# Optimization experiments

Measured on AMD Instinct MI355X. Metric: run time of the kernel, lower is better.

The kernel has to match this reference:

```python
import jax, jax.numpy as jnp
import numpy as np

TEMPERATURE = 0.1  # InfoNCE default
K_POS, K_NEG = 5, 10


def _l2norm(x, eps):
    return x / jnp.maximum(jnp.linalg.norm(x, axis=-1, keepdims=True), eps)


def setup_inputs() -> dict:
    key = jax.random.key(0)
    k1, k2 = jax.random.split(key)
    anchor = jax.random.normal(k1, (4096, 512), dtype=jnp.float32)
    sample = jax.random.normal(k2, (4096, 512), dtype=jnp.float32)
    return {"anchor": anchor, "sample": sample}


def reference(anchor, sample):
    N = anchor.shape[0]
    # Pairwise cosine similarity (torch.cosine_similarity eps=1e-8), computed
    a = _l2norm(anchor, 1e-8)
    sim = a @ a.T  # (N, N)

    # topk largest=True (5 nearest) and largest=False (10 farthest)
    _, pos_idx = jax.lax.top_k(sim, K_POS)    # (N, 5)
    _, neg_idx = jax.lax.top_k(-sim, K_NEG)   # (N, 10), ascending sim

    # Faithful replication of the original gather/repeat pattern:
    # query = sample.repeat(5, 1) -> tiling (index i maps to sample[i % N])
    query = jnp.tile(sample, (K_POS, 1))                          # (5N, d)
    pos = sample[pos_idx.reshape(-1)]                             # (5N, d) anchor-major
    neg = sample[neg_idx.reshape(-1)].reshape(N, K_NEG, -1)       # (N, 10, d)
    neg = jnp.repeat(neg, K_POS, axis=0)                          # (5N, 10, d)

    # InfoNCE (negative_mode='paired'): F.normalize (eps=1e-12) then logits.
    q = _l2norm(query, 1e-12)
    p = _l2norm(pos, 1e-12)
    n = _l2norm(neg, 1e-12)
    pos_logit = jnp.sum(q * p, axis=1, keepdims=True)             # (5N, 1)
    neg_logits = jnp.einsum('bd,bkd->bk', q, n)                   # (5N, 10)
    logits = jnp.concatenate([pos_logit, neg_logits], axis=1) / TEMPERATURE
    # cross_entropy with labels == 0, mean reduction
    loss = -jnp.mean(jax.nn.log_softmax(logits, axis=1)[:, 0])
    return loss
```

## Files before the change

kernel.cpp:

```cpp
#include <hip/hip_runtime.h>
#include <math.h>

#define N 4096
#define D 512
#define KPOS 5
#define KNEG 10
#define NB 32
#define NPAIR (NB * (NB - 1) / 2)
#define NJOB 1024

typedef short s16x8 __attribute__((ext_vector_type(8)));
typedef unsigned short u16x8 __attribute__((ext_vector_type(8)));
typedef float f32x4 __attribute__((ext_vector_type(4)));

__device__ __forceinline__ unsigned short f2bf(float x) {
    unsigned u = __float_as_uint(x);
    unsigned r = (u + 0x7FFFu + ((u >> 16) & 1u)) >> 16;
    return (unsigned short)r;
}
__device__ __forceinline__ float bf2f(unsigned short b) {
    return __uint_as_float(((unsigned)b) << 16);
}
__device__ __forceinline__ unsigned short mapbf(float x) {
    const unsigned short h = f2bf(x);
    return h ^ ((h & 0x8000u) ? 0xFFFFu : 0x8000u);
}
__device__ __forceinline__ unsigned umax_(unsigned a, unsigned b) { return a > b ? a : b; }
__device__ __forceinline__ unsigned umin_(unsigned a, unsigned b) { return a < b ? a : b; }

__global__ __launch_bounds__(256) void norm_kernel(const float* __restrict__ anchor,
                                                   const float* __restrict__ sample,
                                                   unsigned short* __restrict__ Abf,
                                                   unsigned short* __restrict__ s_norm) {
    const int wave = threadIdx.x >> 6, lane = threadIdx.x & 63;
    const int row = blockIdx.x * 4 + wave;
    const bool is_anchor = row < N;
    const float* in = is_anchor ? anchor + (size_t)row * D
                                : sample + (size_t)(row - N) * D;
    const float eps = is_anchor ? 1e-8f : 1e-12f;

    const float4 v0 = *(const float4*)&in[lane * 4];
    const float4 v1 = *(const float4*)&in[256 + lane * 4];
    float ss = v0.x * v0.x + v0.y * v0.y + v0.z * v0.z + v0.w * v0.w
             + v1.x * v1.x + v1.y * v1.y + v1.z * v1.z + v1.w * v1.w;
#pragma unroll
    for (int off = 32; off > 0; off >>= 1) ss += __shfl_xor(ss, off);
    const float inv = 1.0f / fmaxf(sqrtf(ss), eps);

    unsigned short* out = is_anchor ? Abf + (size_t)row * D
                                    : s_norm + (size_t)(row - N) * D;
    ushort4 o0, o1;
    o0.x = f2bf(v0.x * inv); o0.y = f2bf(v0.y * inv);
    o0.z = f2bf(v0.z * inv); o0.w = f2bf(v0.w * inv);
    o1.x = f2bf(v1.x * inv); o1.y = f2bf(v1.y * inv);
    o1.z = f2bf(v1.z * inv); o1.w = f2bf(v1.w * inv);
    *(ushort4*)&out[lane * 4] = o0;
    *(ushort4*)&out[256 + lane * 4] = o1;
}

#define ATILE (128 * 64)
#define BTILE (64 * 64)

__device__ __forceinline__ void stage_ab(const unsigned short* __restrict__ A,
                                         unsigned short* As, unsigned short* Bs,
                                         int rowA, int colB, int kl, int t) {
#pragma unroll
    for (int i = 0; i < 4; ++i) {
        const int c = i * 256 + t;
        const int r = c >> 3;
        const int ke = ((c & 7) ^ (r & 7)) * 8;
        __builtin_amdgcn_global_load_lds(
            (const __attribute__((address_space(1))) void*)(A + (size_t)(rowA + r) * D + kl + ke),
            (__attribute__((address_space(3))) void*)(As + c * 8), 16, 0, 0);
    }
#pragma unroll
    for (int i = 0; i < 2; ++i) {
        const int c = i * 256 + t;
        const int r = c >> 3;
        const int ke = ((c & 7) ^ (r & 7)) * 8;
        __builtin_amdgcn_global_load_lds(
            (const __attribute__((address_space(1))) void*)(A + (size_t)(colB + r) * D + kl + ke),
            (__attribute__((address_space(3))) void*)(Bs + c * 8), 16, 0, 0);
    }
}

__global__ __launch_bounds__(256) void gemm_bf16(const unsigned short* __restrict__ Abf,
                                                 unsigned short* __restrict__ C) {
    const int q = (blockIdx.x % 8) * (NJOB / 8) + blockIdx.x / 8;

    int bi, bj, h;
    if (q < 2 * NPAIR) {
        const int op = q >> 1;
        h = q & 1;
        bi = (int)(31.5f - sqrtf(31.5f * 31.5f - 2.f * (float)op));
        while (31 * bi - bi * (bi - 1) / 2 > op) --bi;
        while (31 * (bi + 1) - (bi + 1) * bi / 2 <= op) ++bi;
        bj = bi + 1 + (op - (31 * bi - bi * (bi - 1) / 2));
    } else {
        const int d = q - 2 * NPAIR;
        bi = bj = d >> 1;
        h = d & 1;
    }

    __shared__ __align__(16) unsigned short As[2 * ATILE];
    __shared__ __align__(16) unsigned short Bs[2 * BTILE];

    const int t = threadIdx.x;
    const int l = t & 63;
    const int w = t >> 6;
    const int wr = w >> 1, wc = w & 1;
    const int rowA = bi * 128;
    const int colB = bj * 128 + h * 64;
    const int lrow = l & 15, lgrp = l >> 4;

    f32x4 acc[4][2];
#pragma unroll
    for (int m = 0; m < 4; ++m)
#pragma unroll
        for (int n = 0; n < 2; ++n) acc[m][n] = (f32x4){0.f, 0.f, 0.f, 0.f};

    stage_ab(Abf, As, Bs, rowA, colB, 0, t);
    __syncthreads();

    for (int kc = 0; kc < 8; ++kc) {
        const int cur = kc & 1;
        if (kc < 7)
            stage_ab(Abf, As + (cur ^ 1) * ATILE, Bs + (cur ^ 1) * BTILE,
                     rowA, colB, (kc + 1) * 64, t);

        const char* AsB = (const char*)(As + cur * ATILE);
        const char* BsB = (const char*)(Bs + cur * BTILE);
#pragma unroll
        for (int kk = 0; kk < 2; ++kk) {
            s16x8 af[4], bfr[2];
#pragma unroll
            for (int m = 0; m < 4; ++m) {
                const int row = wr * 64 + m * 16 + lrow;
                af[m] = *(const s16x8*)(AsB + row * 128 + (((kk * 4 + lgrp) ^ (row & 7)) * 16));
            }
#pragma unroll
            for (int n = 0; n < 2; ++n) {
                const int row = wc * 32 + n * 16 + lrow;
                bfr[n] = *(const s16x8*)(BsB + row * 128 + (((kk * 4 + lgrp) ^ (row & 7)) * 16));
            }
#pragma unroll
            for (int m = 0; m < 4; ++m)
#pragma unroll
                for (int n = 0; n < 2; ++n)
                    acc[m][n] = __builtin_amdgcn_mfma_f32_16x16x32_bf16(af[m], bfr[n], acc[m][n], 0, 0, 0);
        }
        __syncthreads();
    }

#pragma unroll
    for (int m = 0; m < 4; ++m) {
#pragma unroll
        for (int n = 0; n < 2; ++n) {
            const int col = colB + wc * 32 + n * 16 + lrow;
            const int row0 = rowA + wr * 64 + m * 16 + lgrp * 4;
#pragma unroll
            for (int j = 0; j < 4; ++j)
                C[(size_t)(row0 + j) * N + col] = mapbf(acc[m][n][j]);
        }
    }
    if (bi != bj) {
#pragma unroll
        for (int m = 0; m < 4; ++m) {
#pragma unroll
            for (int n = 0; n < 2; ++n) {
                const int col = colB + wc * 32 + n * 16 + lrow;
                const int row0 = rowA + wr * 64 + m * 16 + lgrp * 4;
                ushort4 pk;
                pk.x = mapbf(acc[m][n][0]);
                pk.y = mapbf(acc[m][n][1]);
                pk.z = mapbf(acc[m][n][2]);
                pk.w = mapbf(acc[m][n][3]);
                *(ushort4*)&C[(size_t)col * N + row0] = pk;
            }
        }
    }
}

__device__ __forceinline__ void ins_top(unsigned* tk, unsigned c) {
#pragma unroll
    for (int q = 0; q < KPOS - 1; ++q) {
        const unsigned x = umax_(tk[q], c);
        c = umin_(tk[q], c);
        tk[q] = x;
    }
    tk[KPOS - 1] = umax_(tk[KPOS - 1], c);
}
__device__ __forceinline__ void ins_bot(unsigned* bk, unsigned c) {
#pragma unroll
    for (int q = 0; q < KNEG - 1; ++q) {
        const unsigned x = umin_(bk[q], c);
        c = umax_(bk[q], c);
        bk[q] = x;
    }
    bk[KNEG - 1] = umin_(bk[KNEG - 1], c);
}
__device__ __forceinline__ void scan8(const unsigned short* __restrict__ s,
                                      int lane, int e, unsigned* tk, unsigned* bk) {
    const int base = 8 * (lane + 64 * e);
    const u16x8 v8 = *(const u16x8*)&s[base];
#pragma unroll
    for (int j = 0; j < 8; ++j) {
        const unsigned kv = ((unsigned)v8[j]) << 16;
        const int idx = base + j;
        ins_top(tk, kv | (unsigned)(idx ^ 0xFFF));
        ins_bot(bk, kv | (unsigned)idx);
    }
}

__global__ __launch_bounds__(256) void fused_topk_loss(const unsigned short* __restrict__ sim,
                                                       const unsigned short* __restrict__ s_norm,
                                                       float* __restrict__ partials) {
    __shared__ float wsum[4];
    const int wave = threadIdx.x >> 6, lane = threadIdx.x & 63;
    const int ia = blockIdx.x * 4 + wave;
    const unsigned short* s = sim + (size_t)ia * N;
    const int cc = lane & 15;
    const int g = lane >> 4;

    unsigned tkA[KPOS], bkA[KNEG], tkB[KPOS], bkB[KNEG];
#pragma unroll
    for (int q = 0; q < KPOS; ++q) { tkA[q] = 0u; tkB[q] = 0u; }
#pragma unroll
    for (int q = 0; q < KNEG; ++q) { bkA[q] = 0xFFFFFFFFu; bkB[q] = 0xFFFFFFFFu; }

#pragma unroll
    for (int ee = 0; ee < 4; ++ee) {
        scan8(s, lane, 2 * ee, tkA, bkA);
        scan8(s, lane, 2 * ee + 1, tkB, bkB);
    }
#pragma unroll
    for (int q = 0; q < KPOS; ++q) ins_top(tkA, tkB[q]);
#pragma unroll
    for (int q = 0; q < KNEG; ++q) ins_bot(bkA, bkB[q]);

    int rowB = 0;
#pragma unroll
    for (int it = 0; it < KPOS; ++it) {
        unsigned m = tkA[0];
#pragma unroll
        for (int off = 32; off > 0; off >>= 1) m = umax_(m, (unsigned)__shfl_xor((int)m, off));
        if (cc == it) rowB = (int)((m & 0xFFFu) ^ 0xFFFu);
        if (tkA[0] == m) {
#pragma unroll
            for (int q = 0; q < KPOS - 1; ++q) tkA[q] = tkA[q + 1];
            tkA[KPOS - 1] = 0u;
        }
    }
#pragma unroll
    for (int it = 0; it < KNEG; ++it) {
        unsigned m = bkA[0];
#pragma unroll
        for (int off = 32; off > 0; off >>= 1) m = umin_(m, (unsigned)__shfl_xor((int)m, off));
        if (cc == KPOS + it) rowB = (int)(m & 0xFFFu);
        if (bkA[0] == m) {
#pragma unroll
            for (int q = 0; q < KNEG - 1; ++q) bkA[q] = bkA[q + 1];
            bkA[KNEG - 1] = 0xFFFFFFFFu;
        }
    }

    const int rowA = (ia * KPOS + ((cc < KPOS) ? cc : 0)) & (N - 1);
    const unsigned short* pA = s_norm + (size_t)rowA * D + g * 8;
    const unsigned short* pB = s_norm + (size_t)rowB * D + g * 8;

    s16x8 a[16], b[16];
#pragma unroll
    for (int kk = 0; kk < 16; ++kk) {
        a[kk] = *(const s16x8*)(pA + kk * 32);
        b[kk] = *(const s16x8*)(pB + kk * 32);
    }
    __builtin_amdgcn_sched_barrier(0);
    asm volatile("" ::: "memory");

    f32x4 acc = (f32x4){0.f, 0.f, 0.f, 0.f};
#pragma unroll
    for (int kk = 0; kk < 16; ++kk)
        acc = __builtin_amdgcn_mfma_f32_16x16x32_bf16(a[kk], b[kk], acc, 0, 0, 0);

    float lsum = 0.f;
#pragma unroll
    for (int j = 0; j < 4; ++j) {
        const int p = g * 4 + j;
        const float logit = acc[j] * 10.f;
        const bool isneg = (cc >= KPOS) && (cc < 15);
        const bool ispos = (cc == p);
        float x = (ispos || isneg) ? logit : -__builtin_inff();
        float m = x;
#pragma unroll
        for (int off = 1; off < 16; off <<= 1) m = fmaxf(m, __shfl_xor(m, off));
        float e = (ispos || isneg) ? expf(logit - m) : 0.f;
        float sx = e;
#pragma unroll
        for (int off = 1; off < 16; off <<= 1) sx += __shfl_xor(sx, off);
        float l0 = ispos ? logit : 0.f;
#pragma unroll
        for (int off = 1; off < 16; off <<= 1) l0 += __shfl_xor(l0, off);
        if (p < KPOS && ispos) lsum += logf(sx) + m - l0;
    }

#pragma unroll
    for (int off = 32; off > 0; off >>= 1) lsum += __shfl_xor(lsum, off);
    if (lane == 0) wsum[wave] = lsum;
    __syncthreads();
    if (threadIdx.x == 0)
        partials[blockIdx.x] = wsum[0] + wsum[1] + wsum[2] + wsum[3];
}

__global__ __launch_bounds__(256) void reduce_kernel(const float* __restrict__ partials,
                                                     float* __restrict__ out) {
    __shared__ float wsum[4];
    const int wave = threadIdx.x >> 6, lane = threadIdx.x & 63;
    float s = partials[threadIdx.x] + partials[threadIdx.x + 256] +
              partials[threadIdx.x + 512] + partials[threadIdx.x + 768];
#pragma unroll
    for (int off = 32; off > 0; off >>= 1) s += __shfl_xor(s, off);
    if (lane == 0) wsum[wave] = s;
    __syncthreads();
    if (threadIdx.x == 0)
        *out = (wsum[0] + wsum[1] + wsum[2] + wsum[3]) * (1.0f / (float)(N * KPOS));
}

extern "C" void kernel_launch(void* const* d_in, const int* in_sizes, int n_in,
                              void* d_out, int out_size, void* d_ws, size_t ws_size,
                              hipStream_t stream) {
    const float* anchor = (const float*)d_in[0];
    const float* sample = (const float*)d_in[1];
    float* out = (float*)d_out;

    char* ws = (char*)d_ws;
    unsigned short* Abf    = (unsigned short*)ws;
    unsigned short* s_norm = (unsigned short*)(ws + (size_t)4 * 1024 * 1024);
    unsigned short* sim    = (unsigned short*)(ws + (size_t)8 * 1024 * 1024);
    float* partials = (float*)(ws + (size_t)40 * 1024 * 1024);

    norm_kernel<<<2048, 256, 0, stream>>>(anchor, sample, Abf, s_norm);

    gemm_bf16<<<NJOB, 256, 0, stream>>>(Abf, sim);

    fused_topk_loss<<<N / 4, 256, 0, stream>>>(sim, s_norm, partials);

    reduce_kernel<<<1, 256, 0, stream>>>(partials, out);
}
```

Measured before the change: 66.53 us.

## Replace per-element top-k insertion with threshold filtering and LDS candidate compaction

Each wave first computes per-lane packed u16 max/min with v_pk_max/min_u16, then takes the 5th-largest and 10th-smallest lane extremes to get thresholds that bound the true top-5 and bottom-10. Elements that pass a threshold are appended to per-wave LDS candidate buffers via shared atomics, and only those candidates go through the sorting-network insertion. This replaces about 64 full insertions per lane with cheap packed compares. The cost is LDS atomics, a possibly divergent filter step, and a 256-entry candidate cap that could overflow when many values tie.

```diff
diff --git a/kernel.cpp b/kernel.cpp
--- a/kernel.cpp
+++ b/kernel.cpp
@@ -11,6 +11,7 @@
 
 typedef short s16x8 __attribute__((ext_vector_type(8)));
 typedef unsigned short u16x8 __attribute__((ext_vector_type(8)));
+typedef unsigned u32x4 __attribute__((ext_vector_type(4)));
 typedef float f32x4 __attribute__((ext_vector_type(4)));
 
 __device__ __forceinline__ unsigned short f2bf(float x) {
@@ -18,15 +19,18 @@
     unsigned r = (u + 0x7FFFu + ((u >> 16) & 1u)) >> 16;
     return (unsigned short)r;
 }
-__device__ __forceinline__ float bf2f(unsigned short b) {
-    return __uint_as_float(((unsigned)b) << 16);
-}
 __device__ __forceinline__ unsigned short mapbf(float x) {
     const unsigned short h = f2bf(x);
     return h ^ ((h & 0x8000u) ? 0xFFFFu : 0x8000u);
 }
 __device__ __forceinline__ unsigned umax_(unsigned a, unsigned b) { return a > b ? a : b; }
 __device__ __forceinline__ unsigned umin_(unsigned a, unsigned b) { return a < b ? a : b; }
+__device__ __forceinline__ unsigned pkmax(unsigned a, unsigned b) {
+    unsigned r; asm("v_pk_max_u16 %0, %1, %2" : "=v"(r) : "v"(a), "v"(b)); return r;
+}
+__device__ __forceinline__ unsigned pkmin(unsigned a, unsigned b) {
+    unsigned r; asm("v_pk_min_u16 %0, %1, %2" : "=v"(r) : "v"(a), "v"(b)); return r;
+}
 
 __global__ __launch_bounds__(256) void norm_kernel(const float* __restrict__ anchor,
                                                    const float* __restrict__ sample,
@@ -199,68 +203,137 @@
     }
     bk[KNEG - 1] = umin_(bk[KNEG - 1], c);
 }
-__device__ __forceinline__ void scan8(const unsigned short* __restrict__ s,
-                                      int lane, int e, unsigned* tk, unsigned* bk) {
-    const int base = 8 * (lane + 64 * e);
-    const u16x8 v8 = *(const u16x8*)&s[base];
-#pragma unroll
-    for (int j = 0; j < 8; ++j) {
-        const unsigned kv = ((unsigned)v8[j]) << 16;
-        const int idx = base + j;
-        ins_top(tk, kv | (unsigned)(idx ^ 0xFFF));
-        ins_bot(bk, kv | (unsigned)idx);
-    }
-}
 
 __global__ __launch_bounds__(256) void fused_topk_loss(const unsigned short* __restrict__ sim,
                                                        const unsigned short* __restrict__ s_norm,
                                                        float* __restrict__ partials) {
     __shared__ float wsum[4];
+    __shared__ unsigned cand_top[4][256];
+    __shared__ unsigned cand_bot[4][256];
+    __shared__ unsigned cnt[4][2];
     const int wave = threadIdx.x >> 6, lane = threadIdx.x & 63;
     const int ia = blockIdx.x * 4 + wave;
     const unsigned short* s = sim + (size_t)ia * N;
     const int cc = lane & 15;
     const int g = lane >> 4;
 
-    unsigned tkA[KPOS], bkA[KNEG], tkB[KPOS], bkB[KNEG];
-#pragma unroll
-    for (int q = 0; q < KPOS; ++q) { tkA[q] = 0u; tkB[q] = 0u; }
-#pragma unroll
-    for (int q = 0; q < KNEG; ++q) { bkA[q] = 0xFFFFFFFFu; bkB[q] = 0xFFFFFFFFu; }
-
-#pragma unroll
-    for (int ee = 0; ee < 4; ++ee) {
-        scan8(s, lane, 2 * ee, tkA, bkA);
-        scan8(s, lane, 2 * ee + 1, tkB, bkB);
-    }
-#pragma unroll
-    for (int q = 0; q < KPOS; ++q) ins_top(tkA, tkB[q]);
-#pragma unroll
-    for (int q = 0; q < KNEG; ++q) ins_bot(bkA, bkB[q]);
+    if (lane == 0) { cnt[wave][0] = 0u; cnt[wave][1] = 0u; }
+
+    const u32x4 d0 = __builtin_bit_cast(u32x4, *(const u16x8*)&s[8 * lane]);
+    const u32x4 d1 = __builtin_bit_cast(u32x4, *(const u16x8*)&s[8 * (lane + 64)]);
+    const u32x4 d2 = __builtin_bit_cast(u32x4, *(const u16x8*)&s[8 * (lane + 128)]);
+    const u32x4 d3 = __builtin_bit_cast(u32x4, *(const u16x8*)&s[8 * (lane + 192)]);
+    const u32x4 d4 = __builtin_bit_cast(u32x4, *(const u16x8*)&s[8 * (lane + 256)]);
+    const u32x4 d5 = __builtin_bit_cast(u32x4, *(const u16x8*)&s[8 * (lane + 320)]);
+    const u32x4 d6 = __builtin_bit_cast(u32x4, *(const u16x8*)&s[8 * (lane + 384)]);
+    const u32x4 d7 = __builtin_bit_cast(u32x4, *(const u16x8*)&s[8 * (lane + 448)]);
+    __builtin_amdgcn_sched_barrier(0);
+    asm volatile("" ::: "memory");
+
+#define VMAX(v) pkmax(pkmax(v.x, v.y), pkmax(v.z, v.w))
+#define VMIN(v) pkmin(pkmin(v.x, v.y), pkmin(v.z, v.w))
+    unsigned mx = VMAX(d0), mn = VMIN(d0);
+    mx = pkmax(mx, VMAX(d1)); mn = pkmin(mn, VMIN(d1));
+    mx = pkmax(mx, VMAX(d2)); mn = pkmin(mn, VMIN(d2));
+    mx = pkmax(mx, VMAX(d3)); mn = pkmin(mn, VMIN(d3));
+    mx = pkmax(mx, VMAX(d4)); mn = pkmin(mn, VMIN(d4));
+    mx = pkmax(mx, VMAX(d5)); mn = pkmin(mn, VMIN(d5));
+    mx = pkmax(mx, VMAX(d6)); mn = pkmin(mn, VMIN(d6));
+    mx = pkmax(mx, VMAX(d7)); mn = pkmin(mn, VMIN(d7));
+#undef VMAX
+#undef VMIN
+    const unsigned lm = umax_(mx >> 16, mx & 0xFFFFu);
+    const unsigned ln = umin_(mn >> 16, mn & 0xFFFFu);
+
+    unsigned T5, T10;
+    {
+        unsigned cur = (lm << 6) | (unsigned)lane;
+#pragma unroll
+        for (int it = 0; it < KPOS; ++it) {
+            unsigned m = cur;
+#pragma unroll
+            for (int off = 32; off > 0; off >>= 1) m = umax_(m, (unsigned)__shfl_xor((int)m, off));
+            if (it == KPOS - 1) T5 = m >> 6;
+            if (cur == m) cur = 0u;
+        }
+        cur = (ln << 6) | (unsigned)lane;
+#pragma unroll
+        for (int it = 0; it < KNEG; ++it) {
+            unsigned m = cur;
+#pragma unroll
+            for (int off = 32; off > 0; off >>= 1) m = umin_(m, (unsigned)__shfl_xor((int)m, off));
+            if (it == KNEG - 1) T10 = m >> 6;
+            if (cur == m) cur = 0xFFFFFFFFu;
+        }
+    }
+    const unsigned t5g = (T5 == 0u) ? 0u : T5 - 1u;
+    const unsigned t10g = (T10 >= 0xFFFFu) ? 0xFFFFu : T10 + 1u;
+    const unsigned pair5 = t5g * 0x10001u;
+    const unsigned pairA = t10g * 0x10001u;
+
+#define SCAN_DW(dd, base)                                                      \
+    {                                                                          \
+        const unsigned pt = pkmax(dd, pair5);                                  \
+        const unsigned pb = pkmin(dd, pairA);                                  \
+        if (pt != pair5 || pb != pairA) {                                      \
+            const unsigned e0 = (dd) & 0xFFFFu, e1 = (dd) >> 16;               \
+            if (e0 >= T5) { unsigned p = atomicAdd(&cnt[wave][0], 1u);         \
+                cand_top[wave][p & 255u] = (e0 << 16) | (unsigned)((base) ^ 0xFFF); } \
+            if (e1 >= T5) { unsigned p = atomicAdd(&cnt[wave][0], 1u);         \
+                cand_top[wave][p & 255u] = (e1 << 16) | (unsigned)(((base) + 1) ^ 0xFFF); } \
+            if (e0 <= T10) { unsigned p = atomicAdd(&cnt[wave][1], 1u);        \
+                cand_bot[wave][p & 255u] = (e0 << 16) | (unsigned)(base); }    \
+            if (e1 <= T10) { unsigned p = atomicAdd(&cnt[wave][1], 1u);        \
+                cand_bot[wave][p & 255u] = (e1 << 16) | (unsigned)((base) + 1); } \
+        }                                                                      \
+    }
+#define SCAN_VEC(dv, vb)                                                       \
+    SCAN_DW(dv.x, (vb));      SCAN_DW(dv.y, (vb) + 2);                         \
+    SCAN_DW(dv.z, (vb) + 4);  SCAN_DW(dv.w, (vb) + 6);
+    SCAN_VEC(d0, 8 * lane)
+    SCAN_VEC(d1, 8 * (lane + 64))
+    SCAN_VEC(d2, 8 * (lane + 128))
+    SCAN_VEC(d3, 8 * (lane + 192))
+    SCAN_VEC(d4, 8 * (lane + 256))
+    SCAN_VEC(d5, 8 * (lane + 320))
+    SCAN_VEC(d6, 8 * (lane + 384))
+    SCAN_VEC(d7, 8 * (lane + 448))
+#undef SCAN_VEC
+#undef SCAN_DW
+
+    const unsigned ctT = umin_(cnt[wave][0], 256u);
+    const unsigned ctB = umin_(cnt[wave][1], 256u);
+    unsigned tk[KPOS], bk[KNEG];
+#pragma unroll
+    for (int q = 0; q < KPOS; ++q) tk[q] = 0u;
+#pragma unroll
+    for (int q = 0; q < KNEG; ++q) bk[q] = 0xFFFFFFFFu;
+    for (unsigned c = lane; c < ctT; c += 64) ins_top(tk, cand_top[wave][c]);
+    for (unsigned c = lane; c < ctB; c += 64) ins_bot(bk, cand_bot[wave][c]);
 
     int rowB = 0;
 #pragma unroll
     for (int it = 0; it < KPOS; ++it) {
-        unsigned m = tkA[0];
+        unsigned m = tk[0];
 #pragma unroll
         for (int off = 32; off > 0; off >>= 1) m = umax_(m, (unsigned)__shfl_xor((int)m, off));
         if (cc == it) rowB = (int)((m & 0xFFFu) ^ 0xFFFu);
-        if (tkA[0] == m) {
-#pragma unroll
-            for (int q = 0; q < KPOS - 1; ++q) tkA[q] = tkA[q + 1];
-            tkA[KPOS - 1] = 0u;
+        if (tk[0] == m) {
+#pragma unroll
+            for (int q = 0; q < KPOS - 1; ++q) tk[q] = tk[q + 1];
+            tk[KPOS - 1] = 0u;
         }
     }
 #pragma unroll
     for (int it = 0; it < KNEG; ++it) {
-        unsigned m = bkA[0];
+        unsigned m = bk[0];
 #pragma unroll
         for (int off = 32; off > 0; off >>= 1) m = umin_(m, (unsigned)__shfl_xor((int)m, off));
         if (cc == KPOS + it) rowB = (int)(m & 0xFFFu);
-        if (bkA[0] == m) {
-#pragma unroll
-            for (int q = 0; q < KNEG - 1; ++q) bkA[q] = bkA[q + 1];
-            bkA[KNEG - 1] = 0xFFFFFFFFu;
+        if (bk[0] == m) {
+#pragma unroll
+            for (int q = 0; q < KNEG - 1; ++q) bk[q] = bk[q + 1];
+            bk[KNEG - 1] = 0xFFFFFFFFu;
         }
     }
 
```

Measured after the change: 63.64 us. 4.3% less time.
